# Performance work log

Hardware: AMD Instinct MI355X
Metric: run time of the kernel (lower is better)

The kernel has to match this reference:

```python
import jax, jax.numpy as jnp
import numpy as np

SEQ, BATCH, IN_DIM, HID, NQ, TAGS = 2048, 1, 8, 4, 4, 32

# ---- 2x2 gate builders (support batched angle t of shape () or (B,)) ----

def _mat2(a, b, c, d):
    vals = [jnp.asarray(v, jnp.complex64) for v in (a, b, c, d)]
    a, b, c, d = jnp.broadcast_arrays(*vals)
    return jnp.stack([jnp.stack([a, b], -1), jnp.stack([c, d], -1)], -2)

def RZg(t):
    t = jnp.asarray(t, jnp.float32).astype(jnp.complex64)
    return _mat2(jnp.exp(-0.5j * t), 0.0, 0.0, jnp.exp(0.5j * t))

def RYg(t):
    t = jnp.asarray(t, jnp.float32); c = jnp.cos(t / 2); s = jnp.sin(t / 2)
    return _mat2(c, -s, s, c)

def RXg(t):
    t = jnp.asarray(t, jnp.float32); c = jnp.cos(t / 2); s = jnp.sin(t / 2)
    return _mat2(c, -1j * s, -1j * s, c)

def PHg(t):
    t = jnp.asarray(t, jnp.float32)
    return _mat2(jnp.ones_like(t), 0.0, 0.0, jnp.exp(1j * t.astype(jnp.complex64)))

_HAD = jnp.array([[1, 1], [1, -1]], jnp.complex64) / np.float32(np.sqrt(2.0))

# ---- statevector primitives (qubit q little-endian: stride 2^q) ----

def apply_1q(psi, U, q, n):
    B = psi.shape[0]
    psi = psi.reshape(B, 1 << (n - 1 - q), 2, 1 << q)
    if U.ndim == 2:
        out = jnp.einsum('ab,Bxby->Bxay', U, psi)
    else:
        out = jnp.einsum('Bab,Bxby->Bxay', U, psi)
    return out.reshape(B, -1)

def apply_cnot(psi, c, t, n):
    B = psi.shape[0]
    p = psi.reshape((B,) + (2,) * n)
    axc, axt = 1 + (n - 1 - c), 1 + (n - 1 - t)
    p = jnp.moveaxis(p, (axc, axt), (1, 2))
    p = jnp.concatenate([p[:, :1], p[:, 1:, ::-1]], axis=1)  # flip target where control=1
    p = jnp.moveaxis(p, (1, 2), (axc, axt))
    return p.reshape(B, -1)

# ---- QCNN conv / pool two-qubit blocks (faithful to source gate lists) ----

def conv_block(psi, a, b, p, n):
    psi = apply_1q(psi, RZg(-np.pi / 2), b, n)
    psi = apply_cnot(psi, b, a, n)
    psi = apply_1q(psi, RZg(p[0]), a, n)
    psi = apply_1q(psi, RYg(p[1]), b, n)
    psi = apply_cnot(psi, a, b, n)
    psi = apply_1q(psi, RYg(p[2]), b, n)
    psi = apply_cnot(psi, b, a, n)
    psi = apply_1q(psi, RZg(np.pi / 2), a, n)
    return psi

def pool_block(psi, a, b, p, n):
    psi = apply_1q(psi, RZg(-np.pi / 2), b, n)
    psi = apply_cnot(psi, b, a, n)
    psi = apply_1q(psi, RZg(p[0]), a, n)
    psi = apply_1q(psi, RYg(p[1]), b, n)
    psi = apply_cnot(psi, a, b, n)
    psi = apply_1q(psi, RYg(p[2]), b, n)
    return psi

# block wiring exactly as built by conv_layer/pool_layer composed on qubits 0..k
CONV1 = [(0, 1), (2, 3), (4, 5), (6, 7), (1, 2), (3, 4), (5, 6), (7, 0)]
POOL1 = [(0, 4), (1, 5), (2, 6), (3, 7)]
CONV2 = [(0, 1), (2, 3), (1, 2), (3, 0)]
POOL2 = [(0, 2), (1, 3)]
CONV3 = [(0, 1), (1, 0)]
POOL3 = [(0, 1)]

def qcnn_forward(x, w):
    # x: (B,8) inputs, w: (63,) ansatz weights -> (B,) expectation <Z_7>
    B = x.shape[0]
    psi = jnp.zeros((B, 256), jnp.complex64).at[:, 0].set(1.0)
    for q in range(8):  # ZFeatureMap(reps=1): H then P(2*x_q) on each qubit
        psi = apply_1q(psi, _HAD, q, 8)
        psi = apply_1q(psi, PHg(2.0 * x[:, q]), q, 8)
    k = 0
    for blocks, fn in ((CONV1, conv_block), (POOL1, pool_block), (CONV2, conv_block),
                       (POOL2, pool_block), (CONV3, conv_block), (POOL3, pool_block)):
        for (a, b) in blocks:
            psi = fn(psi, a, b, w[k:k + 3], 8)
            k += 3
    probs = psi.real ** 2 + psi.imag ** 2
    # observable 'Z'+'I'*7 in Qiskit big-endian string => Z on qubit 7
    sign7 = 1.0 - 2.0 * ((jnp.arange(256) >> 7) & 1).astype(jnp.float32)
    return probs @ sign7

_SIGNS4 = 1.0 - 2.0 * ((jnp.arange(16)[None, :] >> jnp.arange(4)[:, None]) & 1).astype(jnp.float32)  # (4,16)

def qlayer(angles):
    # angles (B,4): encoder rx + trainable rx fused (RX(a)RX(b)=RX(a+b) on same wire)
    B = angles.shape[0]
    psi = jnp.zeros((B, 16), jnp.complex64).at[:, 0].set(1.0)
    for wq in range(4):
        psi = apply_1q(psi, RXg(angles[:, wq]), wq, 4)
    for (c, t) in ((0, 1), (1, 2), (2, 3), (3, 0)):
        psi = apply_cnot(psi, c, t, 4)
    probs = psi.real ** 2 + psi.imag ** 2
    return probs @ _SIGNS4.T  # (B,4) = <Z_w> per wire

def model_forward(sentence, qcnn_w, Wf, bf, Wi, bi, Wu, bu, Wo, bo, thf, thi, thu, tho, Wt, bt):
    S, B, D = sentence.shape
    q = qcnn_forward(sentence.reshape(S * B, D), qcnn_w).reshape(S, B, 1)
    h0 = jnp.zeros((B, HID), jnp.float32)
    c0 = jnp.zeros((B, HID), jnp.float32)
    Ws = jnp.stack([Wf, Wi, Wu, Wo])        # (4, NQ, 1+HID)
    bs = jnp.stack([bf, bi, bu, bo])        # (4, NQ)
    ths = jnp.stack([thf, thi, thu, tho])   # (4, NQ)

    def step(carry, x):
        h, c = carry
        comb = jnp.concatenate([x, h], axis=1)                         # (B, 1+HID)
        ys = jnp.einsum('gqd,Bd->gBq', Ws, comb) + bs[:, None, :]      # (4,B,NQ)
        z = qlayer((ys + ths[:, None, :]).reshape(4 * B, NQ)).reshape(4, B, NQ)
        f = jax.nn.sigmoid(z[0]); i_ = jax.nn.sigmoid(z[1])
        g = jnp.tanh(z[2]); o = jax.nn.sigmoid(z[3])
        c2 = f * c + i_ * g
        h2 = o * jnp.tanh(c2)
        return (h2, c2), h2

    _, hs = jax.lax.scan(step, (h0, c0), q)    # (S,B,HID)
    logits = hs.reshape(S, -1) @ Wt.T + bt      # batch must be 1 per source view()
    return jax.nn.log_softmax(logits, axis=1)


def setup_inputs() -> dict:
    key = jax.random.key(0)
    ks = jax.random.split(key, 16)
    rn = lambda k, s: jax.random.normal(k, s, jnp.float32)
    return {
        'sentence': rn(ks[0], (SEQ, BATCH, IN_DIM)),
        'qcnn_w': rn(ks[1], (63,)),
        'Wf': rn(ks[2], (NQ, 1 + HID)), 'bf': rn(ks[3], (NQ,)),
        'Wi': rn(ks[4], (NQ, 1 + HID)), 'bi': rn(ks[5], (NQ,)),
        'Wu': rn(ks[6], (NQ, 1 + HID)), 'bu': rn(ks[7], (NQ,)),
        'Wo': rn(ks[8], (NQ, 1 + HID)), 'bo': rn(ks[9], (NQ,)),
        'thf': rn(ks[10], (NQ,)), 'thi': rn(ks[11], (NQ,)),
        'thu': rn(ks[12], (NQ,)), 'tho': rn(ks[13], (NQ,)),
        'Wt': rn(ks[14], (TAGS, HID)), 'bt': rn(ks[15], (TAGS,)),
    }


def reference(sentence, qcnn_w, Wf, bf, Wi, bi, Wu, bu, Wo, bo, thf, thi, thu, tho, Wt, bt):
    return model_forward(sentence, qcnn_w, Wf, bf, Wi, bi, Wu, bu, Wo, bo, thf, thi, thu, tho, Wt, bt)
```

## Files before the change

### kernel.cpp

```cpp
#include <hip/hip_runtime.h>
#include <math.h>


#define MAXS 2048
#define SEG  8
#define WARM 24

__device__ __align__(16) float g_preT[16 * MAXS];

template <int CTRL>
__device__ __forceinline__ float dppf(float x) {
    return __int_as_float(__builtin_amdgcn_update_dpp(
        0, __float_as_int(x), CTRL, 0xF, 0xF, true));
}
#define QP_1032 0xB1
#define QP_2301 0x4E
#define QP_3210 0x1B
#define ROR4  0x124
#define ROR8  0x128
#define ROR12 0x12C

__device__ __forceinline__ float fastrcp(float x) {
    return __builtin_amdgcn_rcpf(x);
}

__constant__ int  cAQ[21] = {0,2,4,6,1,3,5,7, 0,1,2,3, 0,2,1,3, 0,1, 0,1, 0};
__constant__ int  cBQ[21] = {1,3,5,7,2,4,6,0, 4,5,6,7, 1,3,2,0, 2,3, 1,0, 1};
__constant__ int  cCV[21] = {1,1,1,1,1,1,1,1, 0,0,0,0, 1,1,1,1, 0,0, 1,1, 0};

__device__ __forceinline__ float2 cmulacc(float2 acc, float2 u, float2 a) {
    acc.x = fmaf(u.x, a.x, fmaf(-u.y, a.y, acc.x));
    acc.y = fmaf(u.x, a.y, fmaf( u.y, a.x, acc.y));
    return acc;
}

__global__ __launch_bounds__(256) void qcnn_kernel(
    const float* __restrict__ sent, const float* __restrict__ wpar,
    const float* __restrict__ Wf, const float* __restrict__ bfv,
    const float* __restrict__ Wi, const float* __restrict__ bi,
    const float* __restrict__ Wu, const float* __restrict__ bu,
    const float* __restrict__ Wo, const float* __restrict__ bo,
    const float* __restrict__ thf, const float* __restrict__ thi,
    const float* __restrict__ thu, const float* __restrict__ tho, int S)
{
    __shared__ float2 sU[336];
    __shared__ float2 sv[4 * 256];
    const int tid = threadIdx.x;
    const int wid = tid >> 6;
    const int L   = tid & 63;

    if (tid < 21) {
        const int b = tid;
        const float p0 = wpar[3*b], p1 = wpar[3*b+1], p2 = wpar[3*b+2];
        float ur[4][4] = {}, ui[4][4] = {};
        #pragma unroll
        for (int m = 0; m < 4; ++m) ur[m][m] = 1.f;
        auto rzrow = [&](int bm, float t) {
            float ch, sh;
            __sincosf(0.5f*t, &sh, &ch);
            for (int m = 0; m < 4; ++m) {
                float pi_ = (m & bm) ? sh : -sh;
                for (int j = 0; j < 4; ++j) {
                    float r = ur[m][j]*ch - ui[m][j]*pi_;
                    float im = ur[m][j]*pi_ + ui[m][j]*ch;
                    ur[m][j] = r; ui[m][j] = im;
                }
            }
        };
        auto ryrow = [&](int bm, float t) {
            float c, s;
            __sincosf(0.5f*t, &s, &c);
            for (int m0 = 0; m0 < 4; ++m0) {
                if (m0 & bm) continue;
                int m1 = m0 | bm;
                for (int j = 0; j < 4; ++j) {
                    float r0 = ur[m0][j], i0 = ui[m0][j];
                    float r1 = ur[m1][j], i1 = ui[m1][j];
                    ur[m0][j] = c*r0 - s*r1; ui[m0][j] = c*i0 - s*i1;
                    ur[m1][j] = s*r0 + c*r1; ui[m1][j] = s*i0 + c*i1;
                }
            }
        };
        auto swrows = [&](int x, int y) {
            for (int j = 0; j < 4; ++j) {
                float tr = ur[x][j]; ur[x][j] = ur[y][j]; ur[y][j] = tr;
                float ti = ui[x][j]; ui[x][j] = ui[y][j]; ui[y][j] = ti;
            }
        };
        const float PIH = 1.57079632679489662f;
        rzrow(2, -PIH); swrows(2, 3); rzrow(1, p0); ryrow(2, p1);
        swrows(1, 3);   ryrow(2, p2);
        if (cCV[b]) { swrows(2, 3); rzrow(1, PIH); }
        for (int m = 0; m < 4; ++m)
            for (int j = 0; j < 4; ++j)
                sU[(b*4 + m)*4 + j] = make_float2(ur[m][j], ui[m][j]);
    }
    __syncthreads();

    int s = blockIdx.x * 4 + wid;
    const bool live = (s < S);
    if (!live) s = S - 1;

    float xs[8];
    #pragma unroll
    for (int q = 0; q < 8; ++q) xs[q] = sent[s * 8 + q];

    float base = 0.f;
    #pragma unroll
    for (int q = 2; q < 8; ++q)
        if ((L >> (q - 2)) & 1) base += xs[q];
    base *= 2.f;
    float2 r[4];
    #pragma unroll
    for (int k = 0; k < 4; ++k) {
        float ph = base;
        if (k & 1) ph += 2.f * xs[0];
        if (k & 2) ph += 2.f * xs[1];
        float sp, cp;
        __sincosf(ph, &sp, &cp);
        r[k] = make_float2(cp * 0.0625f, sp * 0.0625f);
    }

    float2* mysv = sv + wid * 256;
    int curi0 = L * 4, curma = 1, curmb = 2;

    #pragma unroll
    for (int blk = 0; blk < 21; ++blk) {
        float2 o[4];
        #pragma unroll
        for (int m = 0; m < 4; ++m) {
            float2 acc = make_float2(0.f, 0.f);
            #pragma unroll
            for (int j = 0; j < 4; ++j)
                acc = cmulacc(acc, sU[blk*16 + m*4 + j], r[j]);
            o[m] = acc;
        }
        #pragma unroll
        for (int m = 0; m < 4; ++m) r[m] = o[m];

        if (blk < 20) {
            mysv[curi0         ] = r[0];
            mysv[curi0 + curma ] = r[1];
            mysv[curi0 + curmb ] = r[2];
            mysv[curi0 + curma + curmb] = r[3];
            __builtin_amdgcn_wave_barrier();
            const int a2 = cAQ[blk+1], b2 = cBQ[blk+1];
            const int ma = 1 << a2, mb = 1 << b2;
            const int p  = (a2 < b2) ? a2 : b2;
            const int q  = (a2 < b2) ? b2 : a2;
            const int m1 = (1 << p) - 1;
            const int m2 = (1 << (q - 1)) - 1;
            const int i0 = (L & m1) | ((L & (m2 ^ m1)) << 1) | ((L & ~m2) << 2);
            r[0] = mysv[i0];
            r[1] = mysv[i0 + ma];
            r[2] = mysv[i0 + mb];
            r[3] = mysv[i0 + ma + mb];
            __builtin_amdgcn_wave_barrier();
            curi0 = i0; curma = ma; curmb = mb;
        }
    }

    float pr = fmaf(r[0].x, r[0].x, r[0].y * r[0].y)
             + fmaf(r[1].x, r[1].x, r[1].y * r[1].y)
             + fmaf(r[2].x, r[2].x, r[2].y * r[2].y)
             + fmaf(r[3].x, r[3].x, r[3].y * r[3].y);
    if (L >= 32) pr = -pr;
    #pragma unroll
    for (int off = 32; off > 0; off >>= 1)
        pr += __shfl_xor(pr, off, 64);

    if (live && L < 16) {
        const int g = L >> 2, w = L & 3;
        const float* Wg  = (g == 0) ? Wf  : (g == 1) ? Wi  : (g == 2) ? Wu  : Wo;
        const float* bg  = (g == 0) ? bfv : (g == 1) ? bi  : (g == 2) ? bu  : bo;
        const float* thg = (g == 0) ? thf : (g == 1) ? thi : (g == 2) ? thu : tho;
        g_preT[L * MAXS + s] = Wg[w * 5] * pr + bg[w] + thg[w];
    }
}

__global__ __launch_bounds__(64) void lstm_kernel(
    const float* __restrict__ Wf, const float* __restrict__ Wi,
    const float* __restrict__ Wu, const float* __restrict__ Wo,
    const float* __restrict__ Wt, const float* __restrict__ bt,
    float* __restrict__ out, int S)
{
    __shared__ float sW[128];
    __shared__ float sb[32];
    __shared__ float hseg[SEG][4];

    const int b      = blockIdx.x;
    const int tstart = b * SEG;
    if (tstart >= S) return;
    const int tend = (tstart + SEG < S) ? tstart + SEG : S;
    const int t0   = (tstart >= WARM) ? tstart - WARM : 0;

    const int L   = threadIdx.x;
    const int lid = L & 15;
    const int g   = lid >> 2;
    const int w   = lid & 3;

    sW[L] = Wt[L]; sW[64 + L] = Wt[64 + L];
    if (L < 32) sb[L] = bt[L];

    const float* Wg = (g == 0) ? Wf : (g == 1) ? Wi : (g == 2) ? Wu : Wo;
    const float Wp0 = Wg[w*5 + 1 + (w    )];
    const float Wp1 = Wg[w*5 + 1 + (w ^ 1)];
    const float Wp2 = Wg[w*5 + 1 + (w ^ 2)];
    const float Wp3 = Wg[w*5 + 1 + (w ^ 3)];
    const bool  tg  = (g == 2);
    const float selm = tg ? 2.f : 1.f;
    const float adda = tg ? -1.f : 0.f;

    float pres[32];
    const float4* rowp = (const float4*)(g_preT + lid * MAXS + t0);
    #pragma unroll
    for (int c = 0; c < 8; ++c) {
        float4 v = rowp[c];
        pres[4*c+0] = v.x; pres[4*c+1] = v.y;
        pres[4*c+2] = v.z; pres[4*c+3] = v.w;
    }

    float hs = 0.f, hb1 = 0.f, hb2 = 0.f, hb3 = 0.f;
    float cst = 0.f;

    #pragma unroll
    for (int k = 0; k < WARM + SEG; ++k) {
        const int t = t0 + k;
        float t01 = fmaf(Wp0, hs, Wp1 * hb1);
        float t23 = fmaf(Wp2, hb2, fmaf(Wp3, hb3, pres[k]));
        float th  = t01 + t23;
        float d   = __cosf(th);
        float v1 = dppf<QP_1032>(d);
        float pp = d * v1;
        float v2 = dppf<QP_2301>(pp);
        float z = (w == 0) ? v1 * v2
                : (w == 1) ? pp
                : (w == 2) ? v2 * d
                           : pp * v2;
        float sg = fastrcp(1.f + __expf(-z * selm));
        float a  = fmaf(selm, sg, adda);
        float r4  = dppf<ROR4 >(a);
        float r8  = dppf<ROR8 >(a);
        float r12 = dppf<ROR12>(a);
        float af = (g == 0) ? a : (g == 1) ? r4 : (g == 2) ? r8 : r12;
        float ai = (g == 1) ? a : (g == 2) ? r4 : (g == 3) ? r8 : r12;
        float au = (g == 2) ? a : (g == 3) ? r4 : (g == 0) ? r8 : r12;
        float ao = (g == 3) ? a : (g == 0) ? r4 : (g == 1) ? r8 : r12;
        cst = fmaf(af, cst, ai * au);
        float e2 = __expf(-2.f * cst);
        float hq = ao * fmaf(2.f, fastrcp(1.f + e2), -1.f);
        hs  = hq;
        hb1 = dppf<QP_1032>(hq);
        hb2 = dppf<QP_2301>(hq);
        hb3 = dppf<QP_3210>(hq);
        if (t >= tstart && t < tend) {
            if (L < 4)
                hseg[t - tstart][L] = hs;
        }
    }

    __builtin_amdgcn_wave_barrier();

    if (L < tend - tstart) {
        const int t = tstart + L;
        const float h0 = hseg[L][0], h1 = hseg[L][1];
        const float h2 = hseg[L][2], h3 = hseg[L][3];
        float lg[32];
        float m = -1e30f;
        #pragma unroll
        for (int j = 0; j < 32; ++j) {
            lg[j] = sW[4*j+0]*h0 + sW[4*j+1]*h1 + sW[4*j+2]*h2
                  + sW[4*j+3]*h3 + sb[j];
            m = fmaxf(m, lg[j]);
        }
        float se = 0.f;
        #pragma unroll
        for (int j = 0; j < 32; ++j) se += __expf(lg[j] - m);
        float lse = m + __logf(se);
        #pragma unroll
        for (int j = 0; j < 32; ++j) out[32*t+j] = lg[j] - lse;
    }
}

extern "C" void kernel_launch(void* const* d_in, const int* in_sizes, int n_in,
                              void* d_out, int out_size, void* d_ws, size_t ws_size,
                              hipStream_t stream)
{
    const float* sent = (const float*)d_in[0];
    const float* wq   = (const float*)d_in[1];
    const float* Wf   = (const float*)d_in[2];  const float* bfv = (const float*)d_in[3];
    const float* Wi   = (const float*)d_in[4];  const float* bi  = (const float*)d_in[5];
    const float* Wu   = (const float*)d_in[6];  const float* bu  = (const float*)d_in[7];
    const float* Wo   = (const float*)d_in[8];  const float* bo  = (const float*)d_in[9];
    const float* thf  = (const float*)d_in[10]; const float* thi = (const float*)d_in[11];
    const float* thu  = (const float*)d_in[12]; const float* tho = (const float*)d_in[13];
    const float* Wt   = (const float*)d_in[14]; const float* bt  = (const float*)d_in[15];

    int S = in_sizes[0] / 8;
    if (S > MAXS) S = MAXS;
    float* outp = (float*)d_out;
    const int nseg = (S + SEG - 1) / SEG;

    qcnn_kernel<<<(S + 3) / 4, 256, 0, stream>>>(sent, wq, Wf, bfv, Wi, bi,
                                                 Wu, bu, Wo, bo,
                                                 thf, thi, thu, tho, S);
    lstm_kernel<<<nseg, 64, 0, stream>>>(Wf, Wi, Wu, Wo, Wt, bt, outp, S);
}
```

Baseline: 101.8 us.

## Fuse QCNN and LSTM kernels into one per-segment kernel with recomputed warmup

Merges the two launches into a single kernel. Each block recomputes the QCNN preactivations for its own 32-step window, including the warmup steps, and keeps them in shared memory, so the global g_preT round trip and the second launch go away. Gate-unitary construction is split across 84 threads instead of 21, and the log-softmax output is parallelised across 256 threads with shuffle reductions. In exchange, each QCNN timestep is computed about four times over (the window is 32 steps for 8 outputs), which adds roughly fourfold redundant statevector work.

```diff
diff --git a/kernel.cpp b/kernel.cpp
--- a/kernel.cpp
+++ b/kernel.cpp
@@ -5,8 +5,7 @@
 #define MAXS 2048
 #define SEG  8
 #define WARM 24
-
-__device__ __align__(16) float g_preT[16 * MAXS];
+#define WIN  (WARM + SEG)
 
 template <int CTRL>
 __device__ __forceinline__ float dppf(float x) {
@@ -34,251 +33,251 @@
     return acc;
 }
 
-__global__ __launch_bounds__(256) void qcnn_kernel(
+__global__ __launch_bounds__(256) void fused_kernel(
     const float* __restrict__ sent, const float* __restrict__ wpar,
     const float* __restrict__ Wf, const float* __restrict__ bfv,
     const float* __restrict__ Wi, const float* __restrict__ bi,
     const float* __restrict__ Wu, const float* __restrict__ bu,
     const float* __restrict__ Wo, const float* __restrict__ bo,
     const float* __restrict__ thf, const float* __restrict__ thi,
-    const float* __restrict__ thu, const float* __restrict__ tho, int S)
+    const float* __restrict__ thu, const float* __restrict__ tho,
+    const float* __restrict__ Wt, const float* __restrict__ bt,
+    float* __restrict__ out, int S)
 {
     __shared__ float2 sU[336];
     __shared__ float2 sv[4 * 256];
+    __shared__ float  preA[16][36];
+    __shared__ float  sW[128];
+    __shared__ float  sb[32];
+    __shared__ float  hseg[SEG][4];
+
     const int tid = threadIdx.x;
     const int wid = tid >> 6;
     const int L   = tid & 63;
 
-    if (tid < 21) {
-        const int b = tid;
+    const int blk_b  = blockIdx.x;
+    const int tstart = blk_b * SEG;
+    if (tstart >= S) return;
+    const int tend = (tstart + SEG < S) ? tstart + SEG : S;
+    const int t0   = (tstart >= WARM) ? tstart - WARM : 0;
+
+    if (tid < 84) {
+        const int b = tid >> 2, j = tid & 3;
         const float p0 = wpar[3*b], p1 = wpar[3*b+1], p2 = wpar[3*b+2];
-        float ur[4][4] = {}, ui[4][4] = {};
-        #pragma unroll
-        for (int m = 0; m < 4; ++m) ur[m][m] = 1.f;
-        auto rzrow = [&](int bm, float t) {
-            float ch, sh;
-            __sincosf(0.5f*t, &sh, &ch);
+        float ur[4] = {0.f,0.f,0.f,0.f}, ui[4] = {0.f,0.f,0.f,0.f};
+        ur[j] = 1.f;
+        auto rz = [&](int bm, float ch, float sh) {
+            #pragma unroll
             for (int m = 0; m < 4; ++m) {
                 float pi_ = (m & bm) ? sh : -sh;
-                for (int j = 0; j < 4; ++j) {
-                    float r = ur[m][j]*ch - ui[m][j]*pi_;
-                    float im = ur[m][j]*pi_ + ui[m][j]*ch;
-                    ur[m][j] = r; ui[m][j] = im;
-                }
+                float r  = ur[m]*ch - ui[m]*pi_;
+                float im = ur[m]*pi_ + ui[m]*ch;
+                ur[m] = r; ui[m] = im;
             }
         };
-        auto ryrow = [&](int bm, float t) {
-            float c, s;
-            __sincosf(0.5f*t, &s, &c);
+        auto ry = [&](int bm, float c, float s) {
+            #pragma unroll
             for (int m0 = 0; m0 < 4; ++m0) {
                 if (m0 & bm) continue;
                 int m1 = m0 | bm;
-                for (int j = 0; j < 4; ++j) {
-                    float r0 = ur[m0][j], i0 = ui[m0][j];
-                    float r1 = ur[m1][j], i1 = ui[m1][j];
-                    ur[m0][j] = c*r0 - s*r1; ui[m0][j] = c*i0 - s*i1;
-                    ur[m1][j] = s*r0 + c*r1; ui[m1][j] = s*i0 + c*i1;
-                }
+                float r0 = ur[m0], i0 = ui[m0];
+                float r1 = ur[m1], i1 = ui[m1];
+                ur[m0] = c*r0 - s*r1; ui[m0] = c*i0 - s*i1;
+                ur[m1] = s*r0 + c*r1; ui[m1] = s*i0 + c*i1;
             }
         };
-        auto swrows = [&](int x, int y) {
-            for (int j = 0; j < 4; ++j) {
-                float tr = ur[x][j]; ur[x][j] = ur[y][j]; ur[y][j] = tr;
-                float ti = ui[x][j]; ui[x][j] = ui[y][j]; ui[y][j] = ti;
-            }
+        auto sw = [&](int x, int y) {
+            float tr = ur[x]; ur[x] = ur[y]; ur[y] = tr;
+            float ti = ui[x]; ui[x] = ui[y]; ui[y] = ti;
         };
-        const float PIH = 1.57079632679489662f;
-        rzrow(2, -PIH); swrows(2, 3); rzrow(1, p0); ryrow(2, p1);
-        swrows(1, 3);   ryrow(2, p2);
-        if (cCV[b]) { swrows(2, 3); rzrow(1, PIH); }
+        const float RT = 0.70710678118654752f;
+        float c0,s0,c1,s1,c2,s2;
+        __sincosf(0.5f*p0, &s0, &c0);
+        __sincosf(0.5f*p1, &s1, &c1);
+        __sincosf(0.5f*p2, &s2, &c2);
+        rz(2, RT, -RT);
+        sw(2, 3);
+        rz(1, c0, s0);
+        ry(2, c1, s1);
+        sw(1, 3);
+        ry(2, c2, s2);
+        if (cCV[b]) { sw(2, 3); rz(1, RT, RT); }
+        #pragma unroll
         for (int m = 0; m < 4; ++m)
-            for (int j = 0; j < 4; ++j)
-                sU[(b*4 + m)*4 + j] = make_float2(ur[m][j], ui[m][j]);
+            sU[(b*4 + m)*4 + j] = make_float2(ur[m], ui[m]);
     }
+    if (tid >= 128) sW[tid - 128] = Wt[tid - 128];
+    if (tid >= 96 && tid < 128) sb[tid - 96] = bt[tid - 96];
     __syncthreads();
 
-    int s = blockIdx.x * 4 + wid;
-    const bool live = (s < S);
-    if (!live) s = S - 1;
-
-    float xs[8];
-    #pragma unroll
-    for (int q = 0; q < 8; ++q) xs[q] = sent[s * 8 + q];
-
-    float base = 0.f;
-    #pragma unroll
-    for (int q = 2; q < 8; ++q)
-        if ((L >> (q - 2)) & 1) base += xs[q];
-    base *= 2.f;
-    float2 r[4];
-    #pragma unroll
-    for (int k = 0; k < 4; ++k) {
-        float ph = base;
-        if (k & 1) ph += 2.f * xs[0];
-        if (k & 2) ph += 2.f * xs[1];
-        float sp, cp;
-        __sincosf(ph, &sp, &cp);
-        r[k] = make_float2(cp * 0.0625f, sp * 0.0625f);
-    }
-
-    float2* mysv = sv + wid * 256;
-    int curi0 = L * 4, curma = 1, curmb = 2;
-
-    #pragma unroll
-    for (int blk = 0; blk < 21; ++blk) {
-        float2 o[4];
-        #pragma unroll
-        for (int m = 0; m < 4; ++m) {
-            float2 acc = make_float2(0.f, 0.f);
-            #pragma unroll
-            for (int j = 0; j < 4; ++j)
-                acc = cmulacc(acc, sU[blk*16 + m*4 + j], r[j]);
-            o[m] = acc;
-        }
-        #pragma unroll
-        for (int m = 0; m < 4; ++m) r[m] = o[m];
-
-        if (blk < 20) {
-            mysv[curi0         ] = r[0];
-            mysv[curi0 + curma ] = r[1];
-            mysv[curi0 + curmb ] = r[2];
-            mysv[curi0 + curma + curmb] = r[3];
-            __builtin_amdgcn_wave_barrier();
-            const int a2 = cAQ[blk+1], b2 = cBQ[blk+1];
-            const int ma = 1 << a2, mb = 1 << b2;
-            const int p  = (a2 < b2) ? a2 : b2;
-            const int q  = (a2 < b2) ? b2 : a2;
-            const int m1 = (1 << p) - 1;
-            const int m2 = (1 << (q - 1)) - 1;
-            const int i0 = (L & m1) | ((L & (m2 ^ m1)) << 1) | ((L & ~m2) << 2);
-            r[0] = mysv[i0];
-            r[1] = mysv[i0 + ma];
-            r[2] = mysv[i0 + mb];
-            r[3] = mysv[i0 + ma + mb];
-            __builtin_amdgcn_wave_barrier();
-            curi0 = i0; curma = ma; curmb = mb;
-        }
-    }
-
-    float pr = fmaf(r[0].x, r[0].x, r[0].y * r[0].y)
-             + fmaf(r[1].x, r[1].x, r[1].y * r[1].y)
-             + fmaf(r[2].x, r[2].x, r[2].y * r[2].y)
-             + fmaf(r[3].x, r[3].x, r[3].y * r[3].y);
-    if (L >= 32) pr = -pr;
-    #pragma unroll
-    for (int off = 32; off > 0; off >>= 1)
-        pr += __shfl_xor(pr, off, 64);
-
-    if (live && L < 16) {
-        const int g = L >> 2, w = L & 3;
-        const float* Wg  = (g == 0) ? Wf  : (g == 1) ? Wi  : (g == 2) ? Wu  : Wo;
-        const float* bg  = (g == 0) ? bfv : (g == 1) ? bi  : (g == 2) ? bu  : bo;
-        const float* thg = (g == 0) ? thf : (g == 1) ? thi : (g == 2) ? thu : tho;
-        g_preT[L * MAXS + s] = Wg[w * 5] * pr + bg[w] + thg[w];
-    }
-}
-
-__global__ __launch_bounds__(64) void lstm_kernel(
-    const float* __restrict__ Wf, const float* __restrict__ Wi,
-    const float* __restrict__ Wu, const float* __restrict__ Wo,
-    const float* __restrict__ Wt, const float* __restrict__ bt,
-    float* __restrict__ out, int S)
-{
-    __shared__ float sW[128];
-    __shared__ float sb[32];
-    __shared__ float hseg[SEG][4];
-
-    const int b      = blockIdx.x;
-    const int tstart = b * SEG;
-    if (tstart >= S) return;
-    const int tend = (tstart + SEG < S) ? tstart + SEG : S;
-    const int t0   = (tstart >= WARM) ? tstart - WARM : 0;
-
-    const int L   = threadIdx.x;
     const int lid = L & 15;
     const int g   = lid >> 2;
     const int w   = lid & 3;
-
-    sW[L] = Wt[L]; sW[64 + L] = Wt[64 + L];
-    if (L < 32) sb[L] = bt[L];
-
-    const float* Wg = (g == 0) ? Wf : (g == 1) ? Wi : (g == 2) ? Wu : Wo;
-    const float Wp0 = Wg[w*5 + 1 + (w    )];
-    const float Wp1 = Wg[w*5 + 1 + (w ^ 1)];
-    const float Wp2 = Wg[w*5 + 1 + (w ^ 2)];
-    const float Wp3 = Wg[w*5 + 1 + (w ^ 3)];
-    const bool  tg  = (g == 2);
-    const float selm = tg ? 2.f : 1.f;
-    const float adda = tg ? -1.f : 0.f;
-
-    float pres[32];
-    const float4* rowp = (const float4*)(g_preT + lid * MAXS + t0);
-    #pragma unroll
-    for (int c = 0; c < 8; ++c) {
-        float4 v = rowp[c];
-        pres[4*c+0] = v.x; pres[4*c+1] = v.y;
-        pres[4*c+2] = v.z; pres[4*c+3] = v.w;
+    const float* Wg  = (g == 0) ? Wf  : (g == 1) ? Wi  : (g == 2) ? Wu  : Wo;
+    const float* bg  = (g == 0) ? bfv : (g == 1) ? bi  : (g == 2) ? bu  : bo;
+    const float* thg = (g == 0) ? thf : (g == 1) ? thi : (g == 2) ? thu : tho;
+    const float wsc = Wg[w * 5];
+    const float bth = bg[w] + thg[w];
+
+    float2* mysv = sv + wid * 256;
+
+    #pragma unroll 1
+    for (int j8 = 0; j8 < 8; ++j8) {
+        const int trel = wid * 8 + j8;
+        int s = t0 + trel;
+        if (s >= S) s = S - 1;
+
+        float xs[8];
+        #pragma unroll
+        for (int q = 0; q < 8; ++q) xs[q] = sent[s * 8 + q];
+
+        float base = 0.f;
+        #pragma unroll
+        for (int q = 2; q < 8; ++q)
+            if ((L >> (q - 2)) & 1) base += xs[q];
+        base *= 2.f;
+        float2 r[4];
+        #pragma unroll
+        for (int k = 0; k < 4; ++k) {
+            float ph = base;
+            if (k & 1) ph += 2.f * xs[0];
+            if (k & 2) ph += 2.f * xs[1];
+            float sp, cp;
+            __sincosf(ph, &sp, &cp);
+            r[k] = make_float2(cp * 0.0625f, sp * 0.0625f);
+        }
+
+        int curi0 = L * 4, curma = 1, curmb = 2;
+
+        #pragma unroll
+        for (int blk = 0; blk < 21; ++blk) {
+            float2 o[4];
+            #pragma unroll
+            for (int m = 0; m < 4; ++m) {
+                const float4* Urow = (const float4*)(&sU[blk*16 + m*4]);
+                float4 u01 = Urow[0];
+                float4 u23 = Urow[1];
+                float2 acc = make_float2(0.f, 0.f);
+                acc = cmulacc(acc, make_float2(u01.x, u01.y), r[0]);
+                acc = cmulacc(acc, make_float2(u01.z, u01.w), r[1]);
+                acc = cmulacc(acc, make_float2(u23.x, u23.y), r[2]);
+                acc = cmulacc(acc, make_float2(u23.z, u23.w), r[3]);
+                o[m] = acc;
+            }
+            #pragma unroll
+            for (int m = 0; m < 4; ++m) r[m] = o[m];
+
+            if (blk < 20) {
+                mysv[curi0         ] = r[0];
+                mysv[curi0 + curma ] = r[1];
+                mysv[curi0 + curmb ] = r[2];
+                mysv[curi0 + curma + curmb] = r[3];
+                __builtin_amdgcn_wave_barrier();
+                const int a2 = cAQ[blk+1], b2 = cBQ[blk+1];
+                const int ma = 1 << a2, mb = 1 << b2;
+                const int p  = (a2 < b2) ? a2 : b2;
+                const int q  = (a2 < b2) ? b2 : a2;
+                const int m1 = (1 << p) - 1;
+                const int m2 = (1 << (q - 1)) - 1;
+                const int i0 = (L & m1) | ((L & (m2 ^ m1)) << 1) | ((L & ~m2) << 2);
+                r[0] = mysv[i0];
+                r[1] = mysv[i0 + ma];
+                r[2] = mysv[i0 + mb];
+                r[3] = mysv[i0 + ma + mb];
+                __builtin_amdgcn_wave_barrier();
+                curi0 = i0; curma = ma; curmb = mb;
+            }
+        }
+
+        float pr = fmaf(r[0].x, r[0].x, r[0].y * r[0].y)
+                 + fmaf(r[1].x, r[1].x, r[1].y * r[1].y)
+                 + fmaf(r[2].x, r[2].x, r[2].y * r[2].y)
+                 + fmaf(r[3].x, r[3].x, r[3].y * r[3].y);
+        if (L >= 32) pr = -pr;
+        #pragma unroll
+        for (int off = 32; off > 0; off >>= 1)
+            pr += __shfl_xor(pr, off, 64);
+
+        if (L < 16)
+            preA[L][trel] = wsc * pr + bth;
     }
-
-    float hs = 0.f, hb1 = 0.f, hb2 = 0.f, hb3 = 0.f;
-    float cst = 0.f;
-
-    #pragma unroll
-    for (int k = 0; k < WARM + SEG; ++k) {
-        const int t = t0 + k;
-        float t01 = fmaf(Wp0, hs, Wp1 * hb1);
-        float t23 = fmaf(Wp2, hb2, fmaf(Wp3, hb3, pres[k]));
-        float th  = t01 + t23;
-        float d   = __cosf(th);
-        float v1 = dppf<QP_1032>(d);
-        float pp = d * v1;
-        float v2 = dppf<QP_2301>(pp);
-        float z = (w == 0) ? v1 * v2
-                : (w == 1) ? pp
-                : (w == 2) ? v2 * d
-                           : pp * v2;
-        float sg = fastrcp(1.f + __expf(-z * selm));
-        float a  = fmaf(selm, sg, adda);
-        float r4  = dppf<ROR4 >(a);
-        float r8  = dppf<ROR8 >(a);
-        float r12 = dppf<ROR12>(a);
-        float af = (g == 0) ? a : (g == 1) ? r4 : (g == 2) ? r8 : r12;
-        float ai = (g == 1) ? a : (g == 2) ? r4 : (g == 3) ? r8 : r12;
-        float au = (g == 2) ? a : (g == 3) ? r4 : (g == 0) ? r8 : r12;
-        float ao = (g == 3) ? a : (g == 0) ? r4 : (g == 1) ? r8 : r12;
-        cst = fmaf(af, cst, ai * au);
-        float e2 = __expf(-2.f * cst);
-        float hq = ao * fmaf(2.f, fastrcp(1.f + e2), -1.f);
-        hs  = hq;
-        hb1 = dppf<QP_1032>(hq);
-        hb2 = dppf<QP_2301>(hq);
-        hb3 = dppf<QP_3210>(hq);
-        if (t >= tstart && t < tend) {
-            if (L < 4)
+    __syncthreads();
+
+    if (wid == 0) {
+        const float Wp0 = Wg[w*5 + 1 + (w    )];
+        const float Wp1 = Wg[w*5 + 1 + (w ^ 1)];
+        const float Wp2 = Wg[w*5 + 1 + (w ^ 2)];
+        const float Wp3 = Wg[w*5 + 1 + (w ^ 3)];
+        const bool  tg  = (g == 2);
+        const float selm = tg ? 2.f : 1.f;
+        const float adda = tg ? -1.f : 0.f;
+
+        float pres[WIN];
+        #pragma unroll
+        for (int c = 0; c < WIN/4; ++c) {
+            float4 v = *(const float4*)(&preA[lid][4*c]);
+            pres[4*c+0] = v.x; pres[4*c+1] = v.y;
+            pres[4*c+2] = v.z; pres[4*c+3] = v.w;
+        }
+
+        float hs = 0.f, hb1 = 0.f, hb2 = 0.f, hb3 = 0.f;
+        float cst = 0.f;
+
+        #pragma unroll
+        for (int k = 0; k < WIN; ++k) {
+            const int t = t0 + k;
+            float t01 = fmaf(Wp0, hs, Wp1 * hb1);
+            float t23 = fmaf(Wp2, hb2, fmaf(Wp3, hb3, pres[k]));
+            float th  = t01 + t23;
+            float d   = __cosf(th);
+            float v1 = dppf<QP_1032>(d);
+            float pp = d * v1;
+            float v2 = dppf<QP_2301>(pp);
+            float z = (w == 0) ? v1 * v2
+                    : (w == 1) ? pp
+                    : (w == 2) ? v2 * d
+                               : pp * v2;
+            float sg = fastrcp(1.f + __expf(-z * selm));
+            float a  = fmaf(selm, sg, adda);
+            float r4  = dppf<ROR4 >(a);
+            float r8  = dppf<ROR8 >(a);
+            float r12 = dppf<ROR12>(a);
+            float af = (g == 0) ? a : (g == 1) ? r4 : (g == 2) ? r8 : r12;
+            float ai = (g == 1) ? a : (g == 2) ? r4 : (g == 3) ? r8 : r12;
+            float au = (g == 2) ? a : (g == 3) ? r4 : (g == 0) ? r8 : r12;
+            float ao = (g == 3) ? a : (g == 0) ? r4 : (g == 1) ? r8 : r12;
+            cst = fmaf(af, cst, ai * au);
+            float e2 = __expf(-2.f * cst);
+            float hq = ao * fmaf(2.f, fastrcp(1.f + e2), -1.f);
+            hs  = hq;
+            hb1 = dppf<QP_1032>(hq);
+            hb2 = dppf<QP_2301>(hq);
+            hb3 = dppf<QP_3210>(hq);
+            if (t >= tstart && t < tend && L < 4)
                 hseg[t - tstart][L] = hs;
         }
     }
-
-    __builtin_amdgcn_wave_barrier();
-
-    if (L < tend - tstart) {
-        const int t = tstart + L;
-        const float h0 = hseg[L][0], h1 = hseg[L][1];
-        const float h2 = hseg[L][2], h3 = hseg[L][3];
-        float lg[32];
-        float m = -1e30f;
-        #pragma unroll
-        for (int j = 0; j < 32; ++j) {
-            lg[j] = sW[4*j+0]*h0 + sW[4*j+1]*h1 + sW[4*j+2]*h2
-                  + sW[4*j+3]*h3 + sb[j];
-            m = fmaxf(m, lg[j]);
-        }
-        float se = 0.f;
-        #pragma unroll
-        for (int j = 0; j < 32; ++j) se += __expf(lg[j] - m);
+    __syncthreads();
+
+    {
+        const int row = tid >> 5;
+        const int j   = tid & 31;
+        const int t   = tstart + row;
+        const float h0 = hseg[row][0], h1 = hseg[row][1];
+        const float h2 = hseg[row][2], h3 = hseg[row][3];
+        float lgj = fmaf(sW[4*j+0], h0, fmaf(sW[4*j+1], h1,
+                    fmaf(sW[4*j+2], h2, fmaf(sW[4*j+3], h3, sb[j]))));
+        float m = lgj;
+        #pragma unroll
+        for (int off = 16; off > 0; off >>= 1)
+            m = fmaxf(m, __shfl_xor(m, off, 64));
+        float se = __expf(lgj - m);
+        #pragma unroll
+        for (int off = 16; off > 0; off >>= 1)
+            se += __shfl_xor(se, off, 64);
         float lse = m + __logf(se);
-        #pragma unroll
-        for (int j = 0; j < 32; ++j) out[32*t+j] = lg[j] - lse;
+        if (t < tend)
+            out[32*t + j] = lgj - lse;
     }
 }
 
@@ -301,8 +300,8 @@
     float* outp = (float*)d_out;
     const int nseg = (S + SEG - 1) / SEG;
 
-    qcnn_kernel<<<(S + 3) / 4, 256, 0, stream>>>(sent, wq, Wf, bfv, Wi, bi,
-                                                 Wu, bu, Wo, bo,
-                                                 thf, thi, thu, tho, S);
-    lstm_kernel<<<nseg, 64, 0, stream>>>(Wf, Wi, Wu, Wo, Wt, bt, outp, S);
-}
+    fused_kernel<<<nseg, 256, 0, stream>>>(sent, wq, Wf, bfv, Wi, bi,
+                                           Wu, bu, Wo, bo,
+                                           thf, thi, thu, tho,
+                                           Wt, bt, outp, S);
+}
```

New measurement: 135.8 us. +33.4%, slower.
